# Performance work log

Hardware: AMD Instinct MI355X
Metric: run time of the kernel (lower is better)

## Reference

```python
import jax, jax.numpy as jnp
import numpy as np

EPS_TOTAL = 1e-6
EPS_LOG = 1e-7


def setup_inputs() -> dict:
    key = jax.random.key(0)
    k1, k2 = jax.random.split(key)
    z = jax.random.normal(k1, (16, 4096, 64), dtype=jnp.float32)
    codebook = jax.random.normal(k2, (1024, 64), dtype=jnp.float32)
    return {"z": z, "codebook": codebook}


def reference(z, codebook):
    # z: [B, T, C]; codebook: [K, C]. Eval-mode forward (mask=None).
    B, T, C = z.shape
    K = codebook.shape[0]
    x = z.reshape(-1, C)  # [N, C]

    # quantize: squared-distance matrix via matmul + argmin (fp32 math)
    d = ((x * x).sum(-1, keepdims=True)
         - 2.0 * (x @ codebook.T)
         + (codebook * codebook).sum(-1)[None, :])  # [N, K]
    code_idx = jnp.argmin(d, axis=-1)  # [N]

    # dequantize: gather codewords
    z_q = codebook[code_idx]  # [N, C]

    # commitment loss: MSE to detached codewords, mean over tokens
    per_tok = ((x - jax.lax.stop_gradient(z_q)) ** 2).mean(-1)  # [N]
    commit_loss = per_tok.mean()

    # straight-through estimator
    z_q_bar = x + jax.lax.stop_gradient(z_q - x)

    # compute_perplexity metrics (eval path): one-hot scatter histogram
    counts = jnp.zeros((K,), dtype=x.dtype).at[code_idx].add(1.0)
    total = jnp.maximum(counts.sum(), EPS_TOTAL)
    prob = counts / total
    ppl = jnp.exp(-(prob * jnp.log(prob + EPS_LOG)).sum())
    usage = (counts >= 1.0).astype(x.dtype).mean()

    return z_q_bar.reshape(B, T, C), commit_loss, ppl, usage
```

## Files before the change

kernel.cpp:

```cpp
#include <hip/hip_runtime.h>


typedef _Float16 half8 __attribute__((ext_vector_type(8)));
typedef float f32x4 __attribute__((ext_vector_type(4)));

#define NTOK 65536
#define KCODE 1024
#define OUT_SCALARS 4194304
#define MARGIN 1e-3f

#define WS_CNT   1024
#define WS_LOSS  2048
#define WS_CBHL  20480

static __device__ __forceinline__ unsigned int order_key(float f) {
    unsigned int u = __float_as_uint(f);
    unsigned int mask = (u >> 31) ? 0xFFFFFFFFu : 0x80000000u;
    return u ^ mask;
}
static __device__ __forceinline__ float key_to_float(unsigned int k) {
    unsigned int u = (k & 0x80000000u) ? (k ^ 0x80000000u) : ~k;
    return __uint_as_float(u);
}
static __device__ __forceinline__ unsigned long long umin64(unsigned long long a,
                                                            unsigned long long b) {
    return a < b ? a : b;
}
static __device__ __forceinline__ unsigned long long umax64(unsigned long long a,
                                                            unsigned long long b) {
    return a > b ? a : b;
}

__global__ void prep_kernel(const float* __restrict__ cb, float* __restrict__ ws) {
    const int k = blockIdx.x * 256 + threadIdx.x;
    const float4* cb4 = (const float4*)cb;
    float s = 0.f;
#pragma unroll
    for (int j = 0; j < 16; ++j) {
        float4 v = cb4[k * 16 + j];
        s = fmaf(v.x, v.x, s);
        s = fmaf(v.y, v.y, s);
        s = fmaf(v.z, v.z, s);
        s = fmaf(v.w, v.w, s);
    }
    ws[k] = s;
    ws[WS_CNT + k] = 0.f;

    _Float16* base = (_Float16*)(ws + WS_CBHL) + (size_t)(k >> 4) * 2048 + (k & 15) * 64;
    const int c = k & 15;
#pragma unroll
    for (int d8 = 0; d8 < 8; ++d8) {
        float4 a = cb4[k * 16 + 2 * d8], b = cb4[k * 16 + 2 * d8 + 1];
        float xf[8] = {a.x, a.y, a.z, a.w, b.x, b.y, b.z, b.w};
        half8 h, lo;
#pragma unroll
        for (int i = 0; i < 8; ++i) {
            _Float16 hi = (_Float16)xf[i];
            h[i] = hi;
            lo[i] = (_Float16)((xf[i] - (float)hi) * 4096.f);
        }
        const int pos = ((d8 + c) & 7) * 8;
        *(half8*)(base + pos) = h;
        *(half8*)(base + 1024 + pos) = lo;
    }
}

__launch_bounds__(256, 4)
__global__ void quant_kernel(const float* __restrict__ z,
                             const float* __restrict__ cb,
                             float* __restrict__ out,
                             float* __restrict__ ws) {
    const int t = threadIdx.x, blk = blockIdx.x;
    const int w = t >> 6, l = t & 63;
    const int cl = l & 15, g = l >> 4;
    const int tok0 = blk * 64;
    const int tokL = w * 16 + cl;
    const int tokG = tok0 + tokL;

    __shared__ __align__(16) _Float16 tiles[3][2][2048];
    __shared__ __align__(16) float cn_lds[1024];
    __shared__ int win[64];
    __shared__ float lsum[64];

    *(float4*)&cn_lds[t * 4] = *(const float4*)(ws + t * 4);

    half8 zh[2], zl[2];
    {
        const float4* z4 = (const float4*)z + (size_t)tokG * 16;
#pragma unroll
        for (int q = 0; q < 2; ++q) {
            float4 a = z4[2 * g + 8 * q], b = z4[2 * g + 8 * q + 1];
            float xf[8] = {a.x, a.y, a.z, a.w, b.x, b.y, b.z, b.w};
#pragma unroll
            for (int i = 0; i < 8; ++i) {
                _Float16 h = (_Float16)xf[i];
                zh[q][i] = h;
                zl[q][i] = (_Float16)((xf[i] - (float)h) * 4096.f);
            }
        }
    }

    asm volatile("s_waitcnt vmcnt(0) lgkmcnt(0)" ::: "memory");
    __builtin_amdgcn_sched_barrier(0);

    const char* dma_src = (const char*)(ws + WS_CBHL) + w * 1024 + l * 16;
    const int rot = (g + cl) & 7;
    const int o0 = cl * 64 + rot * 8;
    const int o1 = cl * 64 + (rot ^ 4) * 8;

#pragma unroll
    for (int p = 0; p < 2; ++p)
#pragma unroll
        for (int u = 0; u < 2; ++u)
            __builtin_amdgcn_global_load_lds(
                (const __attribute__((address_space(1))) void*)(dma_src + (p * 2 + u) * 4096),
                (__attribute__((address_space(3))) void*)&tiles[p][u][w * 512], 16, 0, 0);

    unsigned long long K1r = ~0ull, K2r = ~0ull;

#define TILE_COMPUTE(ti, TP)                                                          \
    {                                                                                 \
        const _Float16* tp = (TP);                                                    \
        half8 H0 = *(const half8*)(tp + o0);                                          \
        half8 H1 = *(const half8*)(tp + o1);                                          \
        half8 L0 = *(const half8*)(tp + 1024 + o0);                                   \
        half8 L1 = *(const half8*)(tp + 1024 + o1);                                   \
        float4 cnv = *(const float4*)&cn_lds[(ti) * 16 + 4 * g];                      \
        const float cna[4] = {cnv.x, cnv.y, cnv.z, cnv.w};                            \
        f32x4 a1 = {0.f,0.f,0.f,0.f}, a2 = {0.f,0.f,0.f,0.f};                         \
        a1 = __builtin_amdgcn_mfma_f32_16x16x32_f16(H0, zh[0], a1, 0, 0, 0);          \
        a1 = __builtin_amdgcn_mfma_f32_16x16x32_f16(H1, zh[1], a1, 0, 0, 0);          \
        a2 = __builtin_amdgcn_mfma_f32_16x16x32_f16(H0, zl[0], a2, 0, 0, 0);          \
        a2 = __builtin_amdgcn_mfma_f32_16x16x32_f16(H1, zl[1], a2, 0, 0, 0);          \
        a2 = __builtin_amdgcn_mfma_f32_16x16x32_f16(L0, zh[0], a2, 0, 0, 0);          \
        a2 = __builtin_amdgcn_mfma_f32_16x16x32_f16(L1, zh[1], a2, 0, 0, 0);          \
        unsigned long long kk[4];                                                     \
        _Pragma("unroll")                                                             \
        for (int r = 0; r < 4; ++r) {                                                 \
            float dot = fmaf(a2[r], 2.44140625e-4f, a1[r]);                           \
            float d = fmaf(-2.f, dot, cna[r]);                  \
            kk[r] = ((unsigned long long)order_key(d) << 32)                          \
                    | (unsigned)((ti) * 16 + 4 * g + r);                              \
        }                                                                             \
                               \
        unsigned long long lo01 = umin64(kk[0], kk[1]);                               \
        unsigned long long hi01 = umax64(kk[0], kk[1]);                               \
        unsigned long long lo23 = umin64(kk[2], kk[3]);                               \
        unsigned long long hi23 = umax64(kk[2], kk[3]);                               \
        unsigned long long m1 = umin64(lo01, lo23);                                   \
        unsigned long long m2 = umin64(umax64(lo01, lo23), umin64(hi01, hi23));       \
                                                        \
        unsigned long long nlo = umin64(K1r, m1);                                     \
        unsigned long long nhi = umax64(K1r, m1);                                     \
        K2r = umin64(nhi, umin64(K2r, m2));                                           \
        K1r = nlo;                                                                    \
    }

#define PHASE(P, SLOT, SLOT2, VM, ISSUE)                                              \
    {                                                                                 \
        asm volatile("s_waitcnt vmcnt(" VM ")" ::: "memory");                         \
        asm volatile("s_barrier" ::: "memory");                                       \
        if (ISSUE) {                                                                  \
            _Pragma("unroll")                                                         \
            for (int u = 0; u < 2; ++u)                                               \
                __builtin_amdgcn_global_load_lds(                                     \
                    (const __attribute__((address_space(1))) void*)(dma_src + (((P) + 2) * 2 + u) * 4096), \
                    (__attribute__((address_space(3))) void*)&tiles[SLOT2][u][w * 512], \
                    16, 0, 0);                                                        \
        }                                                                             \
        TILE_COMPUTE((P) * 2 + 0, &tiles[SLOT][0][0])                                 \
        TILE_COMPUTE((P) * 2 + 1, &tiles[SLOT][1][0])                                 \
    }

    for (int i3 = 0; i3 < 30; i3 += 3) {
        PHASE(i3 + 0, 0, 2, "4", 1)
        PHASE(i3 + 1, 1, 0, "4", 1)
        PHASE(i3 + 2, 2, 1, "4", 1)
    }
    PHASE(30, 0, 0, "4", 0)
    PHASE(31, 1, 0, "0", 0)
#undef PHASE
#undef TILE_COMPUTE

    unsigned long long k1 = K1r, k2 = K2r;
#pragma unroll
    for (int off = 16; off <= 32; off <<= 1) {
        unsigned long long ok1 = __shfl_xor(k1, off, 64);
        unsigned long long ok2 = __shfl_xor(k2, off, 64);
        unsigned long long lo = umin64(k1, ok1);
        unsigned long long hi = umax64(k1, ok1);
        k2 = umin64(hi, umin64(k2, ok2));
        k1 = lo;
    }

    if (l < 16) {
        int fidx = (int)(unsigned)(k1 & 0xFFFFFFFFull);
        const float d1f = key_to_float((unsigned)(k1 >> 32));
        const float d2f = key_to_float((unsigned)(k2 >> 32));
        if (d2f - d1f < MARGIN) {
            const int ia = fidx;
            const int ib = (int)(unsigned)(k2 & 0xFFFFFFFFull);
            const float4* zr = (const float4*)z + (size_t)tokG * 16;
            const float4* ca = (const float4*)cb + (size_t)ia * 16;
            const float4* cbp = (const float4*)cb + (size_t)ib * 16;
            float sa = 0.f, sb = 0.f;
#pragma unroll
            for (int j = 0; j < 16; ++j) {
                float4 xv = zr[j];
                float4 va = ca[j], vb = cbp[j];
                sa = fmaf(xv.x, va.x, sa); sb = fmaf(xv.x, vb.x, sb);
                sa = fmaf(xv.y, va.y, sa); sb = fmaf(xv.y, vb.y, sb);
                sa = fmaf(xv.z, va.z, sa); sb = fmaf(xv.z, vb.z, sb);
                sa = fmaf(xv.w, va.w, sa); sb = fmaf(xv.w, vb.w, sb);
            }
            const float ea = fmaf(-2.f, sa, cn_lds[ia]);
            const float eb = fmaf(-2.f, sb, cn_lds[ib]);
            const unsigned long long ka = ((unsigned long long)order_key(ea) << 32) | (unsigned)ia;
            const unsigned long long kb = ((unsigned long long)order_key(eb) << 32) | (unsigned)ib;
            fidx = (int)(unsigned)(umin64(ka, kb) & 0xFFFFFFFFull);
        }
        win[tokL] = fidx;
        atomicAdd(&ws[WS_CNT + fidx], 1.f);
    }
    __syncthreads();

    {
        const int tokr = t >> 2, fb = (t & 3) * 4;
        const int idx = win[tokr];
        const float4* zr = (const float4*)z + (size_t)(tok0 + tokr) * 16;
        const float4* cq = (const float4*)cb + (size_t)idx * 16;
        float4* o4 = (float4*)out + (size_t)(tok0 + tokr) * 16;
        float ss = 0.f;
#pragma unroll
        for (int j = 0; j < 4; ++j) {
            float4 xv = zr[fb + j];
            float4 qv = cq[fb + j];
            float4 ov; float dx;
            dx = qv.x - xv.x; ov.x = xv.x + dx; ss = fmaf(dx, dx, ss);
            dx = qv.y - xv.y; ov.y = xv.y + dx; ss = fmaf(dx, dx, ss);
            dx = qv.z - xv.z; ov.z = xv.z + dx; ss = fmaf(dx, dx, ss);
            dx = qv.w - xv.w; ov.w = xv.w + dx; ss = fmaf(dx, dx, ss);
            o4[fb + j] = ov;
        }
        ss += __shfl_down(ss, 2, 64);
        ss += __shfl_down(ss, 1, 64);
        if ((t & 3) == 0) lsum[tokr] = ss * (1.f / 64.f);
    }
    __syncthreads();
    if (t < 64) {
        float v = lsum[t];
#pragma unroll
        for (int off = 32; off > 0; off >>= 1) v += __shfl_down(v, off, 64);
        if (t == 0) ws[WS_LOSS + blk] = v;
    }
}

__global__ void final_kernel(const float* __restrict__ ws, float* __restrict__ out) {
    const int t = threadIdx.x;
    const int l = t & 63, wv = t >> 6;
    __shared__ float rbuf[16];

#define BLOCK_REDUCE(VAR, EXPR)                                             \
    float VAR;                                                              \
    {                                                                       \
        float v_ = (EXPR);                                                  \
        _Pragma("unroll")                                                   \
        for (int off = 32; off > 0; off >>= 1) v_ += __shfl_down(v_, off, 64); \
        if (l == 0) rbuf[wv] = v_;                                          \
        __syncthreads();                                                    \
        float r_ = (t < 16) ? rbuf[t] : 0.f;                                \
        if (wv == 0) {                                                      \
            _Pragma("unroll")                                               \
            for (int off = 8; off > 0; off >>= 1) r_ += __shfl_down(r_, off, 64); \
            if (l == 0) rbuf[0] = r_;                                       \
        }                                                                   \
        __syncthreads();                                                    \
        VAR = rbuf[0];                                                      \
        __syncthreads();                                                    \
    }

    const float c = ws[WS_CNT + t];
    BLOCK_REDUCE(totraw, c)
    const float total = fmaxf(totraw, 1e-6f);
    const float p = c / total;
    BLOCK_REDUCE(ent, p * logf(p + 1e-7f))
    BLOCK_REDUCE(used, (c >= 1.f) ? 1.f : 0.f)
    BLOCK_REDUCE(loss, ws[WS_LOSS + t])
#undef BLOCK_REDUCE

    if (t == 0) {
        out[OUT_SCALARS + 0] = loss * (1.f / (float)NTOK);
        out[OUT_SCALARS + 1] = expf(-ent);
        out[OUT_SCALARS + 2] = used * (1.f / (float)KCODE);
    }
}

extern "C" void kernel_launch(void* const* d_in, const int* in_sizes, int n_in,
                              void* d_out, int out_size, void* d_ws, size_t ws_size,
                              hipStream_t stream) {
    const float* z  = (const float*)d_in[0];
    const float* cb = (const float*)d_in[1];
    float* out = (float*)d_out;
    float* ws  = (float*)d_ws;

    prep_kernel <<<4, 256, 0, stream>>>(cb, ws);
    quant_kernel<<<NTOK / 64, 256, 0, stream>>>(z, cb, out, ws);
    final_kernel<<<1, 1024, 0, stream>>>(ws, out);
}
```

Measured before the change: 88.12 us.

## Split codebook search across two blocks per token group and merge via atomicMin

Each 64-token group is now handled by two blocks, each scanning half the codebook (512 codes), which doubles the grid to fill more compute units. The per-block winners are rescored exactly in fp32 and merged per token with a 64-bit atomicMin into a workspace buffer. Gather, histogram and loss move into a separate gather kernel. The LDS ring becomes four single tiles and launch bounds rise to allow higher occupancy. In exchange it adds a fourth launch, global atomics, and a redundant exact rescore and z re-read per token.

```diff
diff --git a/kernel.cpp b/kernel.cpp
--- a/kernel.cpp
+++ b/kernel.cpp
@@ -12,6 +12,7 @@
 #define WS_CNT   1024
 #define WS_LOSS  2048
 #define WS_CBHL  20480
+#define WS_BESTQ 90112
 
 static __device__ __forceinline__ unsigned int order_key(float f) {
     unsigned int u = __float_as_uint(f);
@@ -32,7 +33,10 @@
 }
 
 __global__ void prep_kernel(const float* __restrict__ cb, float* __restrict__ ws) {
-    const int k = blockIdx.x * 256 + threadIdx.x;
+    const int i = blockIdx.x * 256 + threadIdx.x;
+    ((unsigned long long*)(ws + WS_BESTQ))[i] = ~0ull;
+    if (i >= 1024) return;
+    const int k = i;
     const float4* cb4 = (const float4*)cb;
     float s = 0.f;
 #pragma unroll
@@ -54,10 +58,10 @@
         float xf[8] = {a.x, a.y, a.z, a.w, b.x, b.y, b.z, b.w};
         half8 h, lo;
 #pragma unroll
-        for (int i = 0; i < 8; ++i) {
-            _Float16 hi = (_Float16)xf[i];
-            h[i] = hi;
-            lo[i] = (_Float16)((xf[i] - (float)hi) * 4096.f);
+        for (int i2 = 0; i2 < 8; ++i2) {
+            _Float16 hi = (_Float16)xf[i2];
+            h[i2] = hi;
+            lo[i2] = (_Float16)((xf[i2] - (float)hi) * 4096.f);
         }
         const int pos = ((d8 + c) & 7) * 8;
         *(half8*)(base + pos) = h;
@@ -65,22 +69,21 @@
     }
 }
 
-__launch_bounds__(256, 4)
+__launch_bounds__(256, 7)
 __global__ void quant_kernel(const float* __restrict__ z,
                              const float* __restrict__ cb,
-                             float* __restrict__ out,
                              float* __restrict__ ws) {
     const int t = threadIdx.x, blk = blockIdx.x;
+    const int grp = blk & 1023, split = blk >> 10;
     const int w = t >> 6, l = t & 63;
     const int cl = l & 15, g = l >> 4;
-    const int tok0 = blk * 64;
+    const int tok0 = grp * 64;
     const int tokL = w * 16 + cl;
     const int tokG = tok0 + tokL;
-
-    __shared__ __align__(16) _Float16 tiles[3][2][2048];
+    const int TB = split * 32;
+
+    __shared__ __align__(16) _Float16 ring[4][2048];
     __shared__ __align__(16) float cn_lds[1024];
-    __shared__ int win[64];
-    __shared__ float lsum[64];
 
     *(float4*)&cn_lds[t * 4] = *(const float4*)(ws + t * 4);
 
@@ -103,29 +106,27 @@
     asm volatile("s_waitcnt vmcnt(0) lgkmcnt(0)" ::: "memory");
     __builtin_amdgcn_sched_barrier(0);
 
-    const char* dma_src = (const char*)(ws + WS_CBHL) + w * 1024 + l * 16;
+    const char* dma_src = (const char*)(ws + WS_CBHL) + (size_t)TB * 4096 + w * 1024 + l * 16;
     const int rot = (g + cl) & 7;
     const int o0 = cl * 64 + rot * 8;
     const int o1 = cl * 64 + (rot ^ 4) * 8;
 
 #pragma unroll
-    for (int p = 0; p < 2; ++p)
-#pragma unroll
-        for (int u = 0; u < 2; ++u)
-            __builtin_amdgcn_global_load_lds(
-                (const __attribute__((address_space(1))) void*)(dma_src + (p * 2 + u) * 4096),
-                (__attribute__((address_space(3))) void*)&tiles[p][u][w * 512], 16, 0, 0);
+    for (int p = 0; p < 3; ++p)
+        __builtin_amdgcn_global_load_lds(
+            (const __attribute__((address_space(1))) void*)(dma_src + p * 4096),
+            (__attribute__((address_space(3))) void*)&ring[p][w * 512], 16, 0, 0);
 
     unsigned long long K1r = ~0ull, K2r = ~0ull;
 
-#define TILE_COMPUTE(ti, TP)                                                          \
+#define TILE_COMPUTE(ti, SLOT)                                                        \
     {                                                                                 \
-        const _Float16* tp = (TP);                                                    \
+        const _Float16* tp = &ring[SLOT][0];                                          \
         half8 H0 = *(const half8*)(tp + o0);                                          \
         half8 H1 = *(const half8*)(tp + o1);                                          \
         half8 L0 = *(const half8*)(tp + 1024 + o0);                                   \
         half8 L1 = *(const half8*)(tp + 1024 + o1);                                   \
-        float4 cnv = *(const float4*)&cn_lds[(ti) * 16 + 4 * g];                      \
+        float4 cnv = *(const float4*)&cn_lds[(TB + (ti)) * 16 + 4 * g];               \
         const float cna[4] = {cnv.x, cnv.y, cnv.z, cnv.w};                            \
         f32x4 a1 = {0.f,0.f,0.f,0.f}, a2 = {0.f,0.f,0.f,0.f};                         \
         a1 = __builtin_amdgcn_mfma_f32_16x16x32_f16(H0, zh[0], a1, 0, 0, 0);          \
@@ -140,45 +141,42 @@
             float dot = fmaf(a2[r], 2.44140625e-4f, a1[r]);                           \
             float d = fmaf(-2.f, dot, cna[r]);                  \
             kk[r] = ((unsigned long long)order_key(d) << 32)                          \
-                    | (unsigned)((ti) * 16 + 4 * g + r);                              \
+                    | (unsigned)((TB + (ti)) * 16 + 4 * g + r);                       \
         }                                                                             \
-                               \
         unsigned long long lo01 = umin64(kk[0], kk[1]);                               \
         unsigned long long hi01 = umax64(kk[0], kk[1]);                               \
         unsigned long long lo23 = umin64(kk[2], kk[3]);                               \
         unsigned long long hi23 = umax64(kk[2], kk[3]);                               \
         unsigned long long m1 = umin64(lo01, lo23);                                   \
         unsigned long long m2 = umin64(umax64(lo01, lo23), umin64(hi01, hi23));       \
-                                                        \
         unsigned long long nlo = umin64(K1r, m1);                                     \
         unsigned long long nhi = umax64(K1r, m1);                                     \
         K2r = umin64(nhi, umin64(K2r, m2));                                           \
         K1r = nlo;                                                                    \
     }
 
-#define PHASE(P, SLOT, SLOT2, VM, ISSUE)                                              \
+#define PHASE(T, SLOT, SLOT2, VM, ISSUE)                                              \
     {                                                                                 \
         asm volatile("s_waitcnt vmcnt(" VM ")" ::: "memory");                         \
         asm volatile("s_barrier" ::: "memory");                                       \
-        if (ISSUE) {                                                                  \
-            _Pragma("unroll")                                                         \
-            for (int u = 0; u < 2; ++u)                                               \
-                __builtin_amdgcn_global_load_lds(                                     \
-                    (const __attribute__((address_space(1))) void*)(dma_src + (((P) + 2) * 2 + u) * 4096), \
-                    (__attribute__((address_space(3))) void*)&tiles[SLOT2][u][w * 512], \
-                    16, 0, 0);                                                        \
-        }                                                                             \
-        TILE_COMPUTE((P) * 2 + 0, &tiles[SLOT][0][0])                                 \
-        TILE_COMPUTE((P) * 2 + 1, &tiles[SLOT][1][0])                                 \
-    }
-
-    for (int i3 = 0; i3 < 30; i3 += 3) {
-        PHASE(i3 + 0, 0, 2, "4", 1)
-        PHASE(i3 + 1, 1, 0, "4", 1)
-        PHASE(i3 + 2, 2, 1, "4", 1)
-    }
-    PHASE(30, 0, 0, "4", 0)
-    PHASE(31, 1, 0, "0", 0)
+        if (ISSUE)                                                                    \
+            __builtin_amdgcn_global_load_lds(                                         \
+                (const __attribute__((address_space(1))) void*)(dma_src + ((T) + 3) * 4096), \
+                (__attribute__((address_space(3))) void*)&ring[SLOT2][w * 512],       \
+                16, 0, 0);                                                            \
+        TILE_COMPUTE(T, SLOT)                                                         \
+    }
+
+    for (int i4 = 0; i4 < 28; i4 += 4) {
+        PHASE(i4 + 0, 0, 3, "2", 1)
+        PHASE(i4 + 1, 1, 0, "2", 1)
+        PHASE(i4 + 2, 2, 1, "2", 1)
+        PHASE(i4 + 3, 3, 2, "2", 1)
+    }
+    PHASE(28, 0, 3, "2", 1)
+    PHASE(29, 1, 0, "2", 0)
+    PHASE(30, 2, 0, "1", 0)
+    PHASE(31, 3, 0, "0", 0)
 #undef PHASE
 #undef TILE_COMPUTE
 
@@ -197,10 +195,10 @@
         int fidx = (int)(unsigned)(k1 & 0xFFFFFFFFull);
         const float d1f = key_to_float((unsigned)(k1 >> 32));
         const float d2f = key_to_float((unsigned)(k2 >> 32));
+        const float4* zr = (const float4*)z + (size_t)tokG * 16;
         if (d2f - d1f < MARGIN) {
             const int ia = fidx;
             const int ib = (int)(unsigned)(k2 & 0xFFFFFFFFull);
-            const float4* zr = (const float4*)z + (size_t)tokG * 16;
             const float4* ca = (const float4*)cb + (size_t)ia * 16;
             const float4* cbp = (const float4*)cb + (size_t)ib * 16;
             float sa = 0.f, sb = 0.f;
@@ -219,40 +217,61 @@
             const unsigned long long kb = ((unsigned long long)order_key(eb) << 32) | (unsigned)ib;
             fidx = (int)(unsigned)(umin64(ka, kb) & 0xFFFFFFFFull);
         }
-        win[tokL] = fidx;
-        atomicAdd(&ws[WS_CNT + fidx], 1.f);
-    }
+        {
+            const float4* cw = (const float4*)cb + (size_t)fidx * 16;
+            float s = 0.f;
+#pragma unroll
+            for (int j = 0; j < 16; ++j) {
+                float4 xv = zr[j];
+                float4 cv = cw[j];
+                s = fmaf(xv.x, cv.x, s);
+                s = fmaf(xv.y, cv.y, s);
+                s = fmaf(xv.z, cv.z, s);
+                s = fmaf(xv.w, cv.w, s);
+            }
+            const float e = fmaf(-2.f, s, cn_lds[fidx]);
+            unsigned long long ek = ((unsigned long long)order_key(e) << 32) | (unsigned)fidx;
+            atomicMin((unsigned long long*)(ws + WS_BESTQ) + tokG, ek);
+        }
+    }
+}
+
+__global__ void gather_kernel(const float* __restrict__ z,
+                              const float* __restrict__ cb,
+                              float* __restrict__ out,
+                              float* __restrict__ ws) {
+    const int tok = blockIdx.x * 256 + threadIdx.x;
+    const unsigned long long* bq = (const unsigned long long*)(ws + WS_BESTQ);
+    const int idx = (int)(unsigned)bq[tok];
+
+    atomicAdd(&ws[WS_CNT + idx], 1.0f);
+
+    const float4* z4 = (const float4*)z + (size_t)tok * 16;
+    const float4* cq = (const float4*)cb + (size_t)idx * 16;
+    float4* o4 = (float4*)out + (size_t)tok * 16;
+    float ssum = 0.f;
+#pragma unroll
+    for (int j = 0; j < 16; ++j) {
+        float4 xv = z4[j];
+        float4 qv = cq[j];
+        float4 ov;
+        float dx;
+        dx = qv.x - xv.x; ov.x = xv.x + dx; ssum = fmaf(dx, dx, ssum);
+        dx = qv.y - xv.y; ov.y = xv.y + dx; ssum = fmaf(dx, dx, ssum);
+        dx = qv.z - xv.z; ov.z = xv.z + dx; ssum = fmaf(dx, dx, ssum);
+        dx = qv.w - xv.w; ov.w = xv.w + dx; ssum = fmaf(dx, dx, ssum);
+        o4[j] = ov;
+    }
+
+    float v = ssum * (1.f / 64.f);
+#pragma unroll
+    for (int off = 32; off > 0; off >>= 1) v += __shfl_down(v, off, 64);
+    __shared__ float wsum[4];
+    int lane = threadIdx.x & 63, wid = threadIdx.x >> 6;
+    if (lane == 0) wsum[wid] = v;
     __syncthreads();
-
-    {
-        const int tokr = t >> 2, fb = (t & 3) * 4;
-        const int idx = win[tokr];
-        const float4* zr = (const float4*)z + (size_t)(tok0 + tokr) * 16;
-        const float4* cq = (const float4*)cb + (size_t)idx * 16;
-        float4* o4 = (float4*)out + (size_t)(tok0 + tokr) * 16;
-        float ss = 0.f;
-#pragma unroll
-        for (int j = 0; j < 4; ++j) {
-            float4 xv = zr[fb + j];
-            float4 qv = cq[fb + j];
-            float4 ov; float dx;
-            dx = qv.x - xv.x; ov.x = xv.x + dx; ss = fmaf(dx, dx, ss);
-            dx = qv.y - xv.y; ov.y = xv.y + dx; ss = fmaf(dx, dx, ss);
-            dx = qv.z - xv.z; ov.z = xv.z + dx; ss = fmaf(dx, dx, ss);
-            dx = qv.w - xv.w; ov.w = xv.w + dx; ss = fmaf(dx, dx, ss);
-            o4[fb + j] = ov;
-        }
-        ss += __shfl_down(ss, 2, 64);
-        ss += __shfl_down(ss, 1, 64);
-        if ((t & 3) == 0) lsum[tokr] = ss * (1.f / 64.f);
-    }
-    __syncthreads();
-    if (t < 64) {
-        float v = lsum[t];
-#pragma unroll
-        for (int off = 32; off > 0; off >>= 1) v += __shfl_down(v, off, 64);
-        if (t == 0) ws[WS_LOSS + blk] = v;
-    }
+    if (threadIdx.x == 0)
+        ws[WS_LOSS + blockIdx.x] = wsum[0] + wsum[1] + wsum[2] + wsum[3];
 }
 
 __global__ void final_kernel(const float* __restrict__ ws, float* __restrict__ out) {
@@ -285,7 +304,7 @@
     const float p = c / total;
     BLOCK_REDUCE(ent, p * logf(p + 1e-7f))
     BLOCK_REDUCE(used, (c >= 1.f) ? 1.f : 0.f)
-    BLOCK_REDUCE(loss, ws[WS_LOSS + t])
+    BLOCK_REDUCE(loss, (t < 256) ? ws[WS_LOSS + t] : 0.f)
 #undef BLOCK_REDUCE
 
     if (t == 0) {
@@ -303,7 +322,8 @@
     float* out = (float*)d_out;
     float* ws  = (float*)d_ws;
 
-    prep_kernel <<<4, 256, 0, stream>>>(cb, ws);
-    quant_kernel<<<NTOK / 64, 256, 0, stream>>>(z, cb, out, ws);
-    final_kernel<<<1, 1024, 0, stream>>>(ws, out);
-}
+    prep_kernel  <<<256, 256, 0, stream>>>(cb, ws);
+    quant_kernel <<<2048, 256, 0, stream>>>(z, cb, ws);
+    gather_kernel<<<256, 256, 0, stream>>>(z, cb, out, ws);
+    final_kernel <<<1, 1024, 0, stream>>>(ws, out);
+}
```

Result: slower. 113.1 us (+28.4%).
